# Kernel optimization log

Measured on AMD Instinct MI355X. Metric: run time of the kernel, lower is better.

The kernel has to match this reference:

```python
import jax, jax.numpy as jnp
import numpy as np

B, T, ENC_IN, DEC_IN, U = 32768, 7, 60, 36, 356


def setup_inputs() -> dict:
    key = jax.random.key(0)
    ks = jax.random.split(key, 12)
    s = 0.05  # small weight scale for numerical sanity
    return {
        "x_batch": jax.random.normal(ks[0], (B, T, ENC_IN), jnp.float32),
        "m_batch": jax.random.normal(ks[1], (B, T, DEC_IN), jnp.float32),
        "enc_kernel": jax.random.normal(ks[2], (ENC_IN, 4 * U), jnp.float32) * s,
        "enc_rec_kernel": jax.random.normal(ks[3], (U, 4 * U), jnp.float32) * s,
        "enc_bias": jnp.zeros((4 * U,), jnp.float32),
        "dec_kernel": jax.random.normal(ks[4], (DEC_IN, 4 * U), jnp.float32) * s,
        "dec_rec_kernel": jax.random.normal(ks[5], (U, 4 * U), jnp.float32) * s,
        "dec_bias": jnp.zeros((4 * U,), jnp.float32),
        "W_map": jax.random.normal(ks[6], (T * U, 768), jnp.float32) * s,
        "b_map": jnp.zeros((768,), jnp.float32),
        "W_deep1": jax.random.normal(ks[7], (768, 768), jnp.float32) * s,
        "b_deep1": jnp.zeros((768,), jnp.float32),
        "W_deep2": jax.random.normal(ks[8], (768, 768), jnp.float32) * s,
        "b_deep2": jnp.zeros((768,), jnp.float32),
        "W_out": jax.random.normal(ks[9], (768, 168), jnp.float32) * s,
        "b_out": jnp.zeros((168,), jnp.float32),
    }


def _lstm(x, K, R, b, h0, c0):
    """Keras-style LSTM. x: [B,T,D]. Returns (hs [B,T,U], h_T, c_T).
    Gate order i, f, g(candidate), o; sigmoid recurrent activation, tanh activation."""
    xz = jnp.einsum('btd,dg->btg', x, K) + b  # precompute input projections [B,T,4U]

    def step(carry, xz_t):
        h, c = carry
        z = xz_t + h @ R
        i, f, g, o = jnp.split(z, 4, axis=-1)
        c = jax.nn.sigmoid(f) * c + jax.nn.sigmoid(i) * jnp.tanh(g)
        h = jax.nn.sigmoid(o) * jnp.tanh(c)
        return (h, c), h

    (h, c), hs = jax.lax.scan(step, (h0, c0), jnp.swapaxes(xz, 0, 1))
    return jnp.swapaxes(hs, 0, 1), h, c


def reference(x_batch, m_batch, enc_kernel, enc_rec_kernel, enc_bias,
              dec_kernel, dec_rec_kernel, dec_bias,
              W_map, b_map, W_deep1, b_deep1, W_deep2, b_deep2, W_out, b_out):
    b = x_batch.shape[0]
    z = jnp.zeros((b, U), x_batch.dtype)
    # encoder: only final states used
    _, s_h, s_c = _lstm(x_batch, enc_kernel, enc_rec_kernel, enc_bias, z, z)
    # decoder: full sequence, initialized with encoder states
    decoded, _, _ = _lstm(m_batch, dec_kernel, dec_rec_kernel, dec_bias, s_h, s_c)
    f = decoded.reshape(b, -1)  # [B, 7*356]
    m = jax.nn.relu(f @ W_map + b_map)
    d = jnp.tanh(m @ W_deep1 + b_deep1)
    d = jnp.tanh(d @ W_deep2 + b_deep2)
    return d @ W_out + b_out
```

## Files before the change

### kernel.cpp

```cpp
#include <hip/hip_runtime.h>

typedef unsigned short u16;
typedef __attribute__((ext_vector_type(8))) short short8;
typedef __attribute__((ext_vector_type(4))) float f32x4;

#define B_ROWS 32768
#define T_STEPS 7
#define ENC_INd 60
#define DEC_INd 36
#define UNITS 356
#define KP_LSTM 448
#define H_OFF 64
#define HID 768
#define OUTN 168
#define OUTNP 256
#define KMAP 2688
#define HALF_E 44040192ull
#define WLSTM_E 688128
#define CG_BLK 6144

__device__ __forceinline__ u16 f2b(float f) {
  unsigned u = __builtin_bit_cast(unsigned, f);
  u += 0x7fffu + ((u >> 16) & 1u);
  return (u16)(u >> 16);
}
__device__ __forceinline__ float sigm(float x) { return 1.0f / (1.0f + __expf(-x)); }
__device__ __forceinline__ float tanhfast(float x) { return 2.0f / (1.0f + __expf(-2.0f * x)) - 1.0f; }

__global__ void fill_sentinel(float* __restrict__ out, int n, float v) {
  int i = blockIdx.x * 256 + threadIdx.x;
  int stride = gridDim.x * 256;
  for (; i < n; i += stride) out[i] = v;
}

__global__ void prep_lstm_w(const float* __restrict__ Km, const float* __restrict__ Rm,
                            const float* __restrict__ bias, int in_dim,
                            u16* __restrict__ WT, float* __restrict__ bias_r)
{
  int idx = blockIdx.x * 256 + threadIdx.x;
  if (idx >= WLSTM_E) return;
  int e    = idx & 7;
  int lane = (idx >> 3) & 63;
  int nf   = (idx >> 9) & 3;
  int t1   = idx >> 11;
  int kk   = t1 % 14;
  int g    = t1 / 14;
  int u = g * 16 + (lane & 15);
  int k = kk * 32 + ((lane >> 4) << 3) + e;
  float v = 0.f;
  if (u < UNITS) {
    int oc = nf * UNITS + u;
    if (k < in_dim) v = Km[(size_t)k * 1424 + oc];
    else if (k >= H_OFF && k < H_OFF + UNITS) v = Rm[(size_t)(k - H_OFF) * 1424 + oc];
    if (k == 0) bias_r[(u << 2) + nf] = bias[oc];
  } else if (k == 0) bias_r[(u << 2) + nf] = 0.f;
  WT[idx] = f2b(v);
}

__global__ void prep_map_w(const float* __restrict__ W, u16* __restrict__ WT)
{
  int idx = blockIdx.x * 256 + threadIdx.x;
  if (idx >= HID * KMAP) return;
  int n = idx / KMAP, k = idx - n * KMAP;
  int t = k / 384, kk = k - t * 384;
  float v = (kk < UNITS) ? W[(size_t)(t * UNITS + kk) * HID + n] : 0.f;
  WT[idx] = f2b(v);
}

__global__ void prep_mlp_w(const float* __restrict__ W, int korig, int norig, int kp,
                           u16* __restrict__ WT, int total)
{
  int idx = blockIdx.x * 256 + threadIdx.x;
  if (idx >= total) return;
  int n = idx / kp, k = idx - n * kp;
  float v = (k < korig && n < norig) ? W[(size_t)k * norig + n] : 0.f;
  WT[idx] = f2b(v);
}

__global__ __launch_bounds__(512)
void lstm_persistent(const float* __restrict__ xg, const float* __restrict__ mg,
                     const u16* __restrict__ WTe, const float* __restrict__ bre,
                     const u16* __restrict__ WTd, const float* __restrict__ brd,
                     u16* __restrict__ fbuf,
                     f32x4* __restrict__ cg0, f32x4* __restrict__ cg1, f32x4* __restrict__ cg2)
{
  __shared__ __align__(16) u16 A[2][64][KP_LSTM];

  const int tid = threadIdx.x;
  const int ns = tid >> 6;
  const int lane = tid & 63;
  const int l15 = lane & 15, l4 = lane >> 4;
  const int blk = blockIdx.x;
  const int row0 = blk * 64;

  f32x4* cgb;
  if (blk < 224)      cgb = cg0 + (size_t)blk * CG_BLK;
  else if (blk < 480) cgb = cg1 + (size_t)(blk - 224) * CG_BLK;
  else                cgb = cg2 + (size_t)(blk - 480) * CG_BLK;

  {
    short8 z = {};
    for (int q = tid; q < 6144; q += 512) {
      int buf = q / 3072, rem = q - buf * 3072;
      int row = rem / 48, blkc = 8 + (rem - row * 48);
      *(short8*)&A[buf][row][blkc << 3] = z;
    }
  }

#pragma unroll 1
  for (int s = 0; s < 14; ++s) {
    const u16*  wt = (s < 7) ? WTe : WTd;
    const float* br = (s < 7) ? bre : brd;
    const float* src = (s < 7) ? xg : mg;
    const int in_dim = (s < 7) ? ENC_INd : DEC_INd;
    const int t = (s < 7) ? s : s - 7;
    const int par = s & 1;

    {
      const int row = tid >> 3, cb = tid & 7;
      const float* sp = src + ((size_t)(row0 + row) * T_STEPS + t) * in_dim;
      const int cbs = cb ^ (row & 7);
      short8 vv;
#pragma unroll
      for (int j = 0; j < 8; ++j) {
        const int cc = (cb << 3) + j;
        float v = (cc < in_dim) ? sp[cc] : 0.f;
        vv[j] = (short)f2b(v);
      }
      *(short8*)&A[par][row][cbs << 3] = vv;
    }
    __syncthreads();

#pragma unroll 1
    for (int p = 0; p < 3; ++p) {
      const int g = p * 8 + ns;
      f32x4 acc[4][4] = {};
      const u16* bp = wt + ((size_t)g * 14) * 2048 + (lane << 3);

#pragma unroll 1
      for (int kk = 0; kk < 14; ++kk) {
        short8 bf[4];
#pragma unroll
        for (int nf = 0; nf < 4; ++nf)
          bf[nf] = *(const short8*)(bp + kk * 2048 + (nf << 9));
        const int cbA = (kk << 2) + l4;
        {
          short8 af0[2];
#pragma unroll
          for (int mf = 0; mf < 2; ++mf) {
            const int ra = (mf << 4) + l15;
            const int cbs = (cbA & 56) | ((cbA ^ ra) & 7);
            af0[mf] = *(const short8*)&A[par][ra][cbs << 3];
          }
#pragma unroll
          for (int mf = 0; mf < 2; ++mf)
#pragma unroll
            for (int nf = 0; nf < 4; ++nf)
              acc[mf][nf] = __builtin_amdgcn_mfma_f32_16x16x32_bf16(af0[mf], bf[nf], acc[mf][nf], 0, 0, 0);
        }
        {
          short8 af1[2];
#pragma unroll
          for (int mf = 0; mf < 2; ++mf) {
            const int ra = ((mf + 2) << 4) + l15;
            const int cbs = (cbA & 56) | ((cbA ^ ra) & 7);
            af1[mf] = *(const short8*)&A[par][ra][cbs << 3];
          }
#pragma unroll
          for (int mf = 0; mf < 2; ++mf)
#pragma unroll
            for (int nf = 0; nf < 4; ++nf)
              acc[mf + 2][nf] = __builtin_amdgcn_mfma_f32_16x16x32_bf16(af1[mf], bf[nf], acc[mf + 2][nf], 0, 0, 0);
        }
      }

      const int u = (g << 4) + l15;
      const int ch = H_OFF + u, cbh = ch >> 3, cih = ch & 7;
      float bz[4];
#pragma unroll
      for (int nf = 0; nf < 4; ++nf) bz[nf] = br[(u << 2) + nf];
#pragma unroll
      for (int mf = 0; mf < 4; ++mf) {
        const int ci = (p * 4 + mf) * 512 + tid;
        f32x4 cw;
        if (s > 0) cw = cgb[ci];
        else { cw[0] = 0.f; cw[1] = 0.f; cw[2] = 0.f; cw[3] = 0.f; }
#pragma unroll
        for (int r = 0; r < 4; ++r) {
          const int row = (mf << 4) + (l4 << 2) + r;
          float zi = acc[mf][0][r] + bz[0];
          float zf = acc[mf][1][r] + bz[1];
          float zg = acc[mf][2][r] + bz[2];
          float zo = acc[mf][3][r] + bz[3];
          float ig = sigm(zi), fg = sigm(zf);
          float gg = tanhfast(zg), og = sigm(zo);
          float cn = fg * cw[r] + ig * gg;
          cw[r] = cn;
          float hv = og * tanhfast(cn);
          u16 hb = f2b(hv);
          const int cbs = (cbh & 56) | ((cbh ^ row) & 7);
          A[par ^ 1][row][(cbs << 3) + cih] = hb;
          if (s >= 7) {
            const int grow = row0 + row;
            fbuf[(size_t)(grow >> 14) * HALF_E
                 + ((size_t)(grow & 16383) * T_STEPS + t) * 384 + u] = hb;
          }
        }
        cgb[ci] = cw;
      }
    }
  }
}

template<int MODE>
__global__ __launch_bounds__(256)
void mlp_gemm(const u16* __restrict__ A, int lda, int kp,
              const u16* __restrict__ WT, const float* __restrict__ bias, int nreal,
              u16* __restrict__ outb, float* __restrict__ outf, int ldo)
{
  __shared__ __align__(16) u16 lds_a[128 * 64];
  __shared__ __align__(16) u16 lds_b[128 * 64];
  const int tid = threadIdx.x;
  const int wid = tid >> 6, lane = tid & 63;
  const int wm = (wid >> 1) << 6, wn = (wid & 1) << 6;
  const int l15 = lane & 15, l4 = lane >> 4;
  const int r0 = tid >> 3, c8 = tid & 7;
  const size_t abase = (size_t)blockIdx.x * 128 * lda;
  const size_t bbase = (size_t)blockIdx.y * 128 * kp;

  f32x4 acc[4][4] = {};

  for (int kt = 0; kt < kp; kt += 64) {
#pragma unroll
    for (int p = 0; p < 4; ++p) {
      int r = r0 + p * 32;
      short8 va = *(const short8*)(A + abase + (size_t)r * lda + kt + (c8 << 3));
      *(short8*)&lds_a[(r << 6) + ((c8 ^ (r & 7)) << 3)] = va;
      short8 vb = *(const short8*)(WT + bbase + (size_t)r * kp + kt + (c8 << 3));
      *(short8*)&lds_b[(r << 6) + ((c8 ^ (r & 7)) << 3)] = vb;
    }
    __syncthreads();
#pragma unroll
    for (int kk = 0; kk < 2; ++kk) {
      short8 af[4], bfr[4];
#pragma unroll
      for (int mf = 0; mf < 4; ++mf) {
        int ra = wm + (mf << 4) + l15;
        int cb = (kk << 2) + l4;
        af[mf] = *(const short8*)&lds_a[(ra << 6) + ((cb ^ (ra & 7)) << 3)];
      }
#pragma unroll
      for (int nf = 0; nf < 4; ++nf) {
        int rb = wn + (nf << 4) + l15;
        int cb = (kk << 2) + l4;
        bfr[nf] = *(const short8*)&lds_b[(rb << 6) + ((cb ^ (rb & 7)) << 3)];
      }
#pragma unroll
      for (int mf = 0; mf < 4; ++mf)
#pragma unroll
        for (int nf = 0; nf < 4; ++nf)
          acc[mf][nf] = __builtin_amdgcn_mfma_f32_16x16x32_bf16(af[mf], bfr[nf], acc[mf][nf], 0, 0, 0);
    }
    __syncthreads();
  }

#pragma unroll
  for (int mf = 0; mf < 4; ++mf) {
    int rowb = blockIdx.x * 128 + wm + (mf << 4) + (l4 << 2);
#pragma unroll
    for (int r = 0; r < 4; ++r) {
      int row = rowb + r;
#pragma unroll
      for (int nf = 0; nf < 4; ++nf) {
        int n = blockIdx.y * 128 + wn + (nf << 4) + l15;
        float v = acc[mf][nf][r];
        size_t oi = (size_t)row * ldo + n;
        if (MODE == 3) {
          outb[oi] = f2b(tanhfast(v + bias[n]));
        } else if (MODE == 5) {
          outb[oi] = f2b(fmaxf(v + bias[n], 0.f));
        } else {
          if (n < nreal) outf[oi] = v + bias[n];
        }
      }
    }
  }
}

extern "C" void kernel_launch(void* const* d_in, const int* in_sizes, int n_in,
                              void* d_out, int out_size, void* d_ws, size_t ws_size,
                              hipStream_t stream)
{
  const float* x    = (const float*)d_in[0];
  const float* m    = (const float*)d_in[1];
  const float* ek   = (const float*)d_in[2];
  const float* erk  = (const float*)d_in[3];
  const float* eb   = (const float*)d_in[4];
  const float* dk   = (const float*)d_in[5];
  const float* drk  = (const float*)d_in[6];
  const float* dbi  = (const float*)d_in[7];
  const float* wmap = (const float*)d_in[8];
  const float* bmap = (const float*)d_in[9];
  const float* wd1  = (const float*)d_in[10];
  const float* bd1  = (const float*)d_in[11];
  const float* wd2  = (const float*)d_in[12];
  const float* bd2  = (const float*)d_in[13];
  const float* wout = (const float*)d_in[14];
  const float* bout = (const float*)d_in[15];

  char* ws = (char*)d_ws;
  size_t off = 0;
  auto alloc = [&](size_t bytes) { char* p = ws + off; off += (bytes + 255) & ~(size_t)255; return p; };

  u16*   WT_enc  = (u16*)  alloc((size_t)WLSTM_E * 2);
  u16*   WT_dec  = (u16*)  alloc((size_t)WLSTM_E * 2);
  float* b_enc_r = (float*)alloc((size_t)384 * 4 * 4);
  float* b_dec_r = (float*)alloc((size_t)384 * 4 * 4);
  u16*   WT_map  = (u16*)  alloc((size_t)HID * KMAP * 2);
  u16*   WT_d1   = (u16*)  alloc((size_t)HID * HID * 2);
  u16*   WT_d2   = (u16*)  alloc((size_t)HID * HID * 2);
  u16*   WT_out  = (u16*)  alloc((size_t)OUTNP * HID * 2);
  u16*   m1_h1   = (u16*)  alloc((size_t)16384 * HID * 2);
  u16*   fbuf    = (u16*)  alloc((size_t)2 * HALF_E * 2);
  f32x4* cg2     = (f32x4*)alloc((size_t)32 * CG_BLK * 16);
  const size_t NEED = off;

  if (ws_size < NEED) {
    fill_sentinel<<<256, 256, 0, stream>>>((float*)d_out, out_size, (float)(ws_size >> 20));
    return;
  }

  f32x4* cg0 = (f32x4*)d_out;
  f32x4* cg1 = (f32x4*)m1_h1;

  u16* fb_h0 = fbuf;
  u16* fb_h1 = fbuf + HALF_E;
  u16* m1_h0 = fb_h1;
  u16* m2_h0 = fb_h0;
  u16* m2_h1 = fb_h0 + (size_t)16384 * HID;
  u16* m3_h0 = fb_h1;
  u16* m3_h1 = m1_h1;

  prep_lstm_w<<<(WLSTM_E + 255) / 256, 256, 0, stream>>>(ek, erk, eb, ENC_INd, WT_enc, b_enc_r);
  prep_lstm_w<<<(WLSTM_E + 255) / 256, 256, 0, stream>>>(dk, drk, dbi, DEC_INd, WT_dec, b_dec_r);
  prep_map_w<<<((HID * KMAP) + 255) / 256, 256, 0, stream>>>(wmap, WT_map);
  prep_mlp_w<<<((HID * HID) + 255) / 256, 256, 0, stream>>>(wd1, HID, HID, HID, WT_d1, HID * HID);
  prep_mlp_w<<<((HID * HID) + 255) / 256, 256, 0, stream>>>(wd2, HID, HID, HID, WT_d2, HID * HID);
  prep_mlp_w<<<((OUTNP * HID) + 255) / 256, 256, 0, stream>>>(wout, HID, OUTN, HID, WT_out, OUTNP * HID);

  lstm_persistent<<<512, 512, 0, stream>>>(x, m, WT_enc, b_enc_r, WT_dec, b_dec_r, fbuf,
                                           cg0, cg1, cg2);

  mlp_gemm<5><<<dim3(128, 6), 256, 0, stream>>>(fb_h1, KMAP, KMAP, WT_map, bmap, HID, m1_h1, nullptr, HID);
  mlp_gemm<5><<<dim3(128, 6), 256, 0, stream>>>(fb_h0, KMAP, KMAP, WT_map, bmap, HID, m1_h0, nullptr, HID);
  mlp_gemm<3><<<dim3(128, 6), 256, 0, stream>>>(m1_h0, HID, HID, WT_d1, bd1, HID, m2_h0, nullptr, HID);
  mlp_gemm<3><<<dim3(128, 6), 256, 0, stream>>>(m1_h1, HID, HID, WT_d1, bd1, HID, m2_h1, nullptr, HID);
  mlp_gemm<3><<<dim3(128, 6), 256, 0, stream>>>(m2_h0, HID, HID, WT_d2, bd2, HID, m3_h0, nullptr, HID);
  mlp_gemm<3><<<dim3(128, 6), 256, 0, stream>>>(m2_h1, HID, HID, WT_d2, bd2, HID, m3_h1, nullptr, HID);
  mlp_gemm<4><<<dim3(128, 2), 256, 0, stream>>>(m3_h0, HID, HID, WT_out, bout, OUTN,
                                                nullptr, (float*)d_out, OUTN);
  mlp_gemm<4><<<dim3(128, 2), 256, 0, stream>>>(m3_h1, HID, HID, WT_out, bout, OUTN,
                                                nullptr, (float*)d_out + (size_t)16384 * OUTN, OUTN);
}
```

Baseline: 1.495 ms.

## Stage MLP GEMM tiles via global_load_lds and hoist LSTM cell-state loads

The MLP GEMM now copies A and B tiles from global memory straight into LDS with the global_load_lds builtin, 16 bytes per lane. The XOR swizzle moves from the LDS write address to the global source column, so no tile data passes through registers. In the LSTM kernel, the cell-state loads for each gate block are issued before the K loop so their latency overlaps the MFMAs. The feature-buffer writes become nontemporal stores. This trades extra registers for the hoisted cell state and relies on the per-wave contiguous LDS destination layout matching the swizzle the fragment reads expect.

```diff
diff --git a/kernel.cpp b/kernel.cpp
--- a/kernel.cpp
+++ b/kernel.cpp
@@ -26,6 +26,11 @@
 }
 __device__ __forceinline__ float sigm(float x) { return 1.0f / (1.0f + __expf(-x)); }
 __device__ __forceinline__ float tanhfast(float x) { return 2.0f / (1.0f + __expf(-2.0f * x)) - 1.0f; }
+
+__device__ __forceinline__ void stage16(const u16* g, u16* l) {
+  __builtin_amdgcn_global_load_lds((const __attribute__((address_space(1))) void*)g,
+                                   (__attribute__((address_space(3))) void*)l, 16, 0, 0);
+}
 
 __global__ void fill_sentinel(float* __restrict__ out, int n, float v) {
   int i = blockIdx.x * 256 + threadIdx.x;
@@ -137,6 +142,17 @@
       f32x4 acc[4][4] = {};
       const u16* bp = wt + ((size_t)g * 14) * 2048 + (lane << 3);
 
+      f32x4 cw0, cw1, cw2, cw3;
+      if (s > 0) {
+        const int cib = (p * 4) * 512 + tid;
+        cw0 = cgb[cib];
+        cw1 = cgb[cib + 512];
+        cw2 = cgb[cib + 1024];
+        cw3 = cgb[cib + 1536];
+      } else {
+        cw0 = f32x4{0.f, 0.f, 0.f, 0.f}; cw1 = cw0; cw2 = cw0; cw3 = cw0;
+      }
+
 #pragma unroll 1
       for (int kk = 0; kk < 14; ++kk) {
         short8 bf[4];
@@ -181,10 +197,7 @@
       for (int nf = 0; nf < 4; ++nf) bz[nf] = br[(u << 2) + nf];
 #pragma unroll
       for (int mf = 0; mf < 4; ++mf) {
-        const int ci = (p * 4 + mf) * 512 + tid;
-        f32x4 cw;
-        if (s > 0) cw = cgb[ci];
-        else { cw[0] = 0.f; cw[1] = 0.f; cw[2] = 0.f; cw[3] = 0.f; }
+        f32x4 cw = (mf == 0) ? cw0 : (mf == 1) ? cw1 : (mf == 2) ? cw2 : cw3;
 #pragma unroll
         for (int r = 0; r < 4; ++r) {
           const int row = (mf << 4) + (l4 << 2) + r;
@@ -202,11 +215,12 @@
           A[par ^ 1][row][(cbs << 3) + cih] = hb;
           if (s >= 7) {
             const int grow = row0 + row;
-            fbuf[(size_t)(grow >> 14) * HALF_E
-                 + ((size_t)(grow & 16383) * T_STEPS + t) * 384 + u] = hb;
+            __builtin_nontemporal_store(hb,
+              &fbuf[(size_t)(grow >> 14) * HALF_E
+                    + ((size_t)(grow & 16383) * T_STEPS + t) * 384 + u]);
           }
         }
-        cgb[ci] = cw;
+        cgb[(p * 4 + mf) * 512 + tid] = cw;
       }
     }
   }
@@ -224,7 +238,6 @@
   const int wid = tid >> 6, lane = tid & 63;
   const int wm = (wid >> 1) << 6, wn = (wid & 1) << 6;
   const int l15 = lane & 15, l4 = lane >> 4;
-  const int r0 = tid >> 3, c8 = tid & 7;
   const size_t abase = (size_t)blockIdx.x * 128 * lda;
   const size_t bbase = (size_t)blockIdx.y * 128 * kp;
 
@@ -232,12 +245,14 @@
 
   for (int kt = 0; kt < kp; kt += 64) {
 #pragma unroll
-    for (int p = 0; p < 4; ++p) {
-      int r = r0 + p * 32;
-      short8 va = *(const short8*)(A + abase + (size_t)r * lda + kt + (c8 << 3));
-      *(short8*)&lds_a[(r << 6) + ((c8 ^ (r & 7)) << 3)] = va;
-      short8 vb = *(const short8*)(WT + bbase + (size_t)r * kp + kt + (c8 << 3));
-      *(short8*)&lds_b[(r << 6) + ((c8 ^ (r & 7)) << 3)] = vb;
+    for (int q = 0; q < 4; ++q) {
+      const int u = q * 256 + tid;
+      const int r = u >> 3, cb = u & 7;
+      const int cs = kt + ((cb ^ (r & 7)) << 3);
+      u16* da = &lds_a[(q * 256 + (wid << 6)) * 8];
+      u16* db = &lds_b[(q * 256 + (wid << 6)) * 8];
+      stage16(A + abase + (size_t)r * lda + cs, da);
+      stage16(WT + bbase + (size_t)r * kp + cs, db);
     }
     __syncthreads();
 #pragma unroll
```

Measured after the change: 1.460 ms. 2.4% less time.
